# Kernel tuning notes

Measured on AMD Instinct MI355X. Metric: run time of the kernel, lower is better.

## Reference

```python
import jax, jax.numpy as jnp
import numpy as np


def setup_inputs() -> dict:
    key = jax.random.key(0)
    B, L, d_model, d_state, expand = 2, 2048, 1024, 16, 2
    d_inner = expand * d_model
    ks = jax.random.split(key, 8)
    s = lambda k, shape, scale: jax.random.normal(k, shape, dtype=jnp.float32) * scale
    x = s(ks[0], (B, L, d_model), 1.0)
    W_in = s(ks[1], (d_model, 2 * d_inner), 0.02)     # in_proj (no bias)
    W_delta = s(ks[2], (d_inner, d_inner), 0.02)      # delta_proj weight
    b_delta = s(ks[3], (d_inner,), 0.02)              # delta_proj bias
    W_B = s(ks[4], (d_inner, d_state), 0.02)          # B_proj (no bias)
    W_C = s(ks[5], (d_inner, d_state), 0.02)          # C_proj (no bias)
    # A_log = log(repeat(arange(1, d_state+1), 'n -> d n'))
    A_log = jnp.log(jnp.broadcast_to(
        jnp.arange(1, d_state + 1, dtype=jnp.float32), (d_inner, d_state)))
    D_param = jnp.ones((d_inner,), dtype=jnp.float32)
    W_out = s(ks[6], (d_inner, d_model), 0.02)        # out_proj (no bias)
    return dict(x=x, W_in=W_in, W_delta=W_delta, b_delta=b_delta,
                W_B=W_B, W_C=W_C, A_log=A_log, D_param=D_param, W_out=W_out)


def reference(x, W_in, W_delta, b_delta, W_B, W_C, A_log, D_param, W_out):
    d_inner = W_delta.shape[0]
    # in_proj then split into ssm branch (u) and gate (res)
    x_and_res = x @ W_in                       # (B, L, 2*d_inner)
    u, res = x_and_res[..., :d_inner], x_and_res[..., d_inner:]
    u = jax.nn.silu(u)                         # (B, L, d_inner)

    # input-dependent SSM parameters
    delta = jax.nn.softplus(u @ W_delta + b_delta)   # (B, L, d_inner)
    Bm = u @ W_B                                     # (B, L, d_state)
    Cm = u @ W_C                                     # (B, L, d_state)
    A = -jnp.exp(A_log)                              # (d_inner, d_state)

    def step(h, inp):
        d_t, B_t, C_t, u_t = inp  # (B,d), (B,n), (B,n), (B,d)
        dA = jnp.exp(d_t[..., None] * A)                          # (B,d,n)
        h = dA * h + d_t[..., None] * B_t[:, None, :] * u_t[..., None]
        y_t = jnp.einsum('bdn,bn->bd', h, C_t)
        return h, y_t

    Bsz = x.shape[0]
    h0 = jnp.zeros((Bsz, d_inner, A.shape[1]), dtype=x.dtype)
    xs = (jnp.swapaxes(delta, 0, 1), jnp.swapaxes(Bm, 0, 1),
          jnp.swapaxes(Cm, 0, 1), jnp.swapaxes(u, 0, 1))
    _, ys = jax.lax.scan(step, h0, xs)          # ys: (L, B, d_inner)
    y = jnp.swapaxes(ys, 0, 1) + u * D_param    # skip connection with D

    y = y * jax.nn.silu(res)                    # gating
    return y @ W_out                            # (B, L, d_model)
```

## Files before the change

### kernel.cpp

```cpp
#include <hip/hip_runtime.h>
#include <hip/hip_bf16.h>

typedef unsigned short ushort_t;
typedef __bf16 bf16x8 __attribute__((ext_vector_type(8)));
typedef float f32x4 __attribute__((ext_vector_type(4)));

typedef const void __attribute__((address_space(1)))* gas1_t;
typedef void __attribute__((address_space(3)))* las3_t;

#define L_SZ 2048
#define DI   2048
#define M_ROWS 4096
#define NC 32
#define TC 64

__device__ __forceinline__ float bf2f(ushort_t u){
  unsigned x = ((unsigned)u) << 16; float f; __builtin_memcpy(&f, &x, 4); return f;
}
__device__ __forceinline__ ushort_t f2bf(float f){
  __hip_bfloat16 h = __float2bfloat16(f);
  ushort_t u; __builtin_memcpy(&u, &h, 2); return u;
}
__device__ __forceinline__ float siluf(float x){ return x / (1.0f + __expf(-x)); }
__device__ __forceinline__ float softplusf(float x){
  return (x > 20.0f) ? x : log1pf(__expf(x));
}

__global__ __launch_bounds__(256) void k_prep(
    const float* __restrict__ W_in, const float* __restrict__ W_delta,
    const float* __restrict__ W_out, const float* __restrict__ W_B,
    const float* __restrict__ W_C, const float* __restrict__ x,
    ushort_t* __restrict__ W_inT, ushort_t* __restrict__ W_bigT,
    ushort_t* __restrict__ W_outT, ushort_t* __restrict__ xb)
{
  int t = blockIdx.x;
  if (t >= 14464){
    int r = 2080 + (t - 14464);
    uint4 z = make_uint4(0,0,0,0);
    *(uint4*)(W_bigT + (size_t)r * 2048 + threadIdx.x * 8) = z;
    return;
  }
  if (t >= 10368){
    size_t i = (size_t)(t - 10368) * 256 + threadIdx.x;
    float4 v = *(const float4*)(x + i * 4);
    ushort_t o[4] = { f2bf(v.x), f2bf(v.y), f2bf(v.z), f2bf(v.w) };
    *(uint2*)(xb + i * 4) = *(const uint2*)o;
    return;
  }
  const float* in; ushort_t* out; int R, C, tx, ty;
  if (t < 4096)      { in=W_in;    out=W_inT;  R=1024; C=4096; tx = t & 127; ty = t >> 7; }
  else if (t < 8192) { t -= 4096;  in=W_delta; out=W_bigT; R=2048; C=2048; tx = t & 63; ty = t >> 6; }
  else if (t < 10240){ t -= 8192;  in=W_out;   out=W_outT; R=2048; C=1024; tx = t & 31; ty = t >> 5; }
  else if (t < 10304){ t -= 10240; in=W_B;  out=W_bigT + (size_t)2048*2048; R=2048; C=16; tx=0; ty=t; }
  else               { t -= 10304; in=W_C;  out=W_bigT + (size_t)2064*2048; R=2048; C=16; tx=0; ty=t; }
  __shared__ ushort_t tile[32][33];
  int c0 = tx * 32, r0 = ty * 32;
  int xx = threadIdx.x & 31, yy = threadIdx.x >> 5;
  #pragma unroll
  for (int i = 0; i < 32; i += 8){
    int r = r0 + yy + i, c = c0 + xx;
    if (r < R && c < C) tile[yy + i][xx] = f2bf(in[(size_t)r * C + c]);
  }
  __syncthreads();
  #pragma unroll
  for (int i = 0; i < 32; i += 8){
    int c = c0 + yy + i, r = r0 + xx;
    if (r < R && c < C) out[(size_t)c * R + r] = tile[xx][yy + i];
  }
}

template<int BM, int BN, int TPB, int WR, int WC, int EPI, int MINW>
__global__ __launch_bounds__(TPB, MINW) void k_gemm2p(
    const ushort_t* __restrict__ A, int lda,
    const ushort_t* __restrict__ Bt, int ldb,
    void* __restrict__ Cout, int ldc,
    const float* __restrict__ bias,
    float* __restrict__ Bm, float* __restrict__ Cm, int K)
{
  constexpr int WM = BM / WR, WN = BN / WC;
  constexpr int MT = WM / 16, NT = WN / 16;
  constexpr int BUFSZ = (BM + BN) * 128;
  constexpr int ACH = BM * 8;
  constexpr int NISSUE = (BM + BN) * 8 / TPB;
  __shared__ __align__(16) char lds[2 * BUFSZ];
  const int tid  = threadIdx.x;
  const int wave = tid >> 6, lane = tid & 63;
  const int quad = lane >> 4, l16 = lane & 15;

  const int gx  = gridDim.x;
  const int nwg = gx * gridDim.y;
  const int bid = blockIdx.y * gx + blockIdx.x;
  const int cpx = nwg >> 3;
  const int wid = (bid & 7) * cpx + (bid >> 3);
  const int bx  = wid % gx, by = wid / gx;

  const int m_blk = by * BM, n_blk = bx * BN;
  const int wm = (wave / WC) * WM, wn = (wave % WC) * WN;

  f32x4 acc[MT][NT] = {};

  const ushort_t* gptr[NISSUE];
  char* lptr[NISSUE];
  #pragma unroll
  for (int i = 0; i < NISSUE; i++){
    int g = tid + i * TPB;
    if (g < ACH){
      int row = g >> 3, c = g & 7;
      gptr[i] = A + (size_t)(m_blk + row) * lda + ((c ^ (row & 7)) * 8);
    } else {
      int gb = g - ACH;
      int row = gb >> 3, c = gb & 7;
      gptr[i] = Bt + (size_t)(n_blk + row) * ldb + ((c ^ (row & 7)) * 8);
    }
    lptr[i] = lds + (size_t)g * 16;
  }

  const int xsw = (l16 & 7);
  const int NSTEP = K >> 6;

  #pragma unroll
  for (int i = 0; i < NISSUE; i++)
    __builtin_amdgcn_global_load_lds((gas1_t)(const void*)gptr[i], (las3_t)lptr[i], 16, 0, 0);
  __syncthreads();

  int cur = 0;
  for (int t = 0; t < NSTEP; ++t){
    if (t + 1 < NSTEP){
      const int nxt = (cur ^ 1) * BUFSZ;
      #pragma unroll
      for (int i = 0; i < NISSUE; i++)
        __builtin_amdgcn_global_load_lds((gas1_t)(const void*)(gptr[i] + (t + 1) * 64),
                                         (las3_t)(lptr[i] + nxt), 16, 0, 0);
    }
    const char* ldsA = lds + cur * BUFSZ;
    const char* ldsB = ldsA + BM * 128;
    #pragma unroll
    for (int s = 0; s < 2; s++){
      const int xa = ((s * 4 + quad) ^ xsw) * 16;
      bf16x8 af[MT], bfr[NT];
      #pragma unroll
      for (int i = 0; i < MT; i++)
        af[i]  = *(const bf16x8*)(ldsA + (wm + i * 16 + l16) * 128 + xa);
      #pragma unroll
      for (int i = 0; i < NT; i++)
        bfr[i] = *(const bf16x8*)(ldsB + (wn + i * 16 + l16) * 128 + xa);
      #pragma unroll
      for (int mt = 0; mt < MT; mt++)
        #pragma unroll
        for (int nt = 0; nt < NT; nt++)
          acc[mt][nt] = __builtin_amdgcn_mfma_f32_16x16x32_bf16(af[mt], bfr[nt], acc[mt][nt], 0, 0, 0);
    }
    __syncthreads();
    cur ^= 1;
  }

  #pragma unroll
  for (int mt = 0; mt < MT; mt++){
    #pragma unroll
    for (int nt = 0; nt < NT; nt++){
      #pragma unroll
      for (int r = 0; r < 4; r++){
        int m = m_blk + wm + mt * 16 + quad * 4 + r;
        int n = n_blk + wn + nt * 16 + l16;
        float v = acc[mt][nt][r];
        if (EPI == 0){
          ((float*)Cout)[(size_t)m * ldc + n] = v;
        } else if (EPI == 1){
          ((__hip_bfloat16*)Cout)[(size_t)m * ldc + n] = __float2bfloat16(siluf(v));
        } else {
          if (n < 2048)      ((ushort_t*)Cout)[(size_t)m * ldc + n] = f2bf(softplusf(v + bias[n]));
          else if (n < 2064) Bm[(size_t)m * 16 + (n - 2048)] = v;
          else if (n < 2080) Cm[(size_t)m * 16 + (n - 2064)] = v;
        }
      }
    }
  }
}

__device__ __forceinline__ void load_An(const float* A_log, int d, float* An){
  const float* ap = A_log + (size_t)d * 16;
  #pragma unroll
  for (int j = 0; j < 16; j += 4){
    float4 v = *(const float4*)(ap + j);
    An[j]   = -__expf(v.x);
    An[j+1] = -__expf(v.y);
    An[j+2] = -__expf(v.z);
    An[j+3] = -__expf(v.w);
  }
}

__global__ __launch_bounds__(256) void k_scan1(
    const ushort_t* __restrict__ delta, const ushort_t* __restrict__ U,
    const float* __restrict__ Bm, const float* __restrict__ A_log,
    float* __restrict__ q, float* __restrict__ S)
{
  __shared__ float ldsB[TC * 16];
  const int tid = threadIdx.x;
  const int ch  = blockIdx.x * 256 + tid;
  const int b   = ch >> 11, d = ch & 2047;
  const int c   = blockIdx.y;
  const int t0  = c * TC;
  {
    int tt = tid >> 2, n4 = (tid & 3) * 4;
    *(float4*)&ldsB[tt * 16 + n4] = *(const float4*)&Bm[((size_t)b * L_SZ + t0 + tt) * 16 + n4];
  }
  float An[16];
  load_An(A_log, d, An);
  __syncthreads();
  float h[16];
  #pragma unroll
  for (int j = 0; j < 16; j++) h[j] = 0.f;
  float Ssum = 0.f;
  const size_t row0 = (size_t)b * L_SZ + t0;
  for (int ti = 0; ti < TC; ti += 8){
    float dlt[8], uv[8];
    #pragma unroll
    for (int k = 0; k < 8; k++){
      size_t row = row0 + ti + k;
      dlt[k] = bf2f(delta[row * DI + d]);
      uv[k]  = bf2f(U[row * 4096 + d]);
    }
    #pragma unroll
    for (int k = 0; k < 8; k++){
      float du = dlt[k] * uv[k];
      Ssum += dlt[k];
      #pragma unroll
      for (int nn = 0; nn < 16; nn++)
        h[nn] = fmaf(__expf(dlt[k] * An[nn]), h[nn], du * ldsB[(ti + k) * 16 + nn]);
    }
  }
  size_t qb = ((size_t)c * M_ROWS + ch) * 16;
  #pragma unroll
  for (int j = 0; j < 16; j += 4)
    *(float4*)&q[qb + j] = make_float4(h[j], h[j+1], h[j+2], h[j+3]);
  S[(size_t)c * M_ROWS + ch] = Ssum;
}

__global__ __launch_bounds__(256) void k_scan_combine(
    const float* __restrict__ q, const float* __restrict__ S,
    const float* __restrict__ A_log, float* __restrict__ hin)
{
  int gid = blockIdx.x * 256 + threadIdx.x;
  int ch = gid >> 4, nn = gid & 15, d = ch & 2047;
  float An = -__expf(A_log[(size_t)d * 16 + nn]);
  float h = 0.f;
  for (int c = 0; c < NC; c++){
    size_t base = (size_t)c * M_ROWS + ch;
    hin[base * 16 + nn] = h;
    h = fmaf(__expf(An * S[base]), h, q[base * 16 + nn]);
  }
}

__global__ __launch_bounds__(256) void k_scan2(
    const ushort_t* __restrict__ delta, const ushort_t* __restrict__ U,
    const float* __restrict__ Bm, const float* __restrict__ Cm,
    const float* __restrict__ A_log, const float* __restrict__ Dpar,
    const float* __restrict__ hin, ushort_t* __restrict__ Y)
{
  __shared__ float ldsBC[TC * 16 * 2];
  const int tid = threadIdx.x;
  const int ch  = blockIdx.x * 256 + tid;
  const int b   = ch >> 11, d = ch & 2047;
  const int c   = blockIdx.y;
  const int t0  = c * TC;
  #pragma unroll
  for (int p = 0; p < 2; p++){
    int tt = (tid >> 3) + p * 32, n2 = (tid & 7) * 2;
    size_t gb = ((size_t)b * L_SZ + t0 + tt) * 16 + n2;
    float2 bv = *(const float2*)&Bm[gb];
    float2 cv = *(const float2*)&Cm[gb];
    float2* dst = (float2*)&ldsBC[(tt * 16 + n2) * 2];
    dst[0] = make_float2(bv.x, cv.x);
    dst[1] = make_float2(bv.y, cv.y);
  }
  float An[16];
  load_An(A_log, d, An);
  float Dv = Dpar[d];
  __syncthreads();
  float h[16];
  size_t hb = ((size_t)c * M_ROWS + ch) * 16;
  #pragma unroll
  for (int j = 0; j < 16; j += 4){
    float4 hv = *(const float4*)&hin[hb + j];
    h[j] = hv.x; h[j+1] = hv.y; h[j+2] = hv.z; h[j+3] = hv.w;
  }
  const size_t row0 = (size_t)b * L_SZ + t0;
  for (int ti = 0; ti < TC; ti += 8){
    float dlt[8], uv[8], sres[8];
    #pragma unroll
    for (int k = 0; k < 8; k++){
      size_t row = row0 + ti + k;
      dlt[k]  = bf2f(delta[row * DI + d]);
      uv[k]   = bf2f(U[row * 4096 + d]);
      sres[k] = bf2f(U[row * 4096 + 2048 + d]);
    }
    ushort_t yo[8];
    #pragma unroll
    for (int k = 0; k < 8; k++){
      float du = dlt[k] * uv[k];
      float y = 0.f;
      #pragma unroll
      for (int nn = 0; nn < 16; nn++){
        float2 bc = *(const float2*)&ldsBC[((ti + k) * 16 + nn) * 2];
        h[nn] = fmaf(__expf(dlt[k] * An[nn]), h[nn], du * bc.x);
        y = fmaf(h[nn], bc.y, y);
      }
      yo[k] = f2bf((y + uv[k] * Dv) * sres[k]);
    }
    #pragma unroll
    for (int k = 0; k < 8; k++)
      Y[(row0 + ti + k) * DI + d] = yo[k];
  }
}

extern "C" void kernel_launch(void* const* d_in, const int* in_sizes, int n_in,
                              void* d_out, int out_size, void* d_ws, size_t ws_size,
                              hipStream_t stream)
{
  const float* x       = (const float*)d_in[0];
  const float* W_in    = (const float*)d_in[1];
  const float* W_delta = (const float*)d_in[2];
  const float* b_delta = (const float*)d_in[3];
  const float* W_B     = (const float*)d_in[4];
  const float* W_C     = (const float*)d_in[5];
  const float* A_log   = (const float*)d_in[6];
  const float* D_par   = (const float*)d_in[7];
  const float* W_out   = (const float*)d_in[8];

  char* ws = (char*)d_ws;
  size_t off = 0;
  auto alloc = [&](size_t bytes){ char* p = ws + off; off += (bytes + 255) & ~(size_t)255; return p; };
  ushort_t* W_inT  = (ushort_t*)alloc((size_t)4096*1024*2);
  ushort_t* W_bigT = (ushort_t*)alloc((size_t)2304*2048*2);
  ushort_t* W_outT = (ushort_t*)alloc((size_t)1024*2048*2);
  ushort_t* xb     = (ushort_t*)alloc((size_t)4096*1024*2);
  ushort_t* U      = (ushort_t*)alloc((size_t)4096*4096*2);
  ushort_t* dl     = (ushort_t*)alloc((size_t)4096*2048*2);
  float*    Bm     = (float*)alloc((size_t)4096*16*4);
  float*    Cm     = (float*)alloc((size_t)4096*16*4);
  float*    qbuf   = (float*)alloc((size_t)NC*4096*16*4);
  float*    Sbuf   = (float*)alloc((size_t)NC*4096*4);
  float*    hin    = (float*)alloc((size_t)NC*4096*16*4);
  ushort_t* Y      = (ushort_t*)alloc((size_t)4096*2048*2);

  k_prep<<<dim3(14560),256,0,stream>>>(W_in, W_delta, W_out, W_B, W_C, x,
                                       W_inT, W_bigT, W_outT, xb);

  k_gemm2p<256,256,512,2,4,1,2><<<dim3(16,16),512,0,stream>>>(
      xb, 1024, W_inT, 1024, U, 4096, nullptr, nullptr, nullptr, 1024);

  k_gemm2p<128,64,256,2,2,2,3><<<dim3(34,32),256,0,stream>>>(
      U, 4096, W_bigT, 2048, dl, 2048, b_delta, Bm, Cm, 2048);

  k_scan1<<<dim3(16,NC),256,0,stream>>>(dl, U, Bm, A_log, qbuf, Sbuf);
  k_scan_combine<<<dim3(256),256,0,stream>>>(qbuf, Sbuf, A_log, hin);
  k_scan2<<<dim3(16,NC),256,0,stream>>>(dl, U, Bm, Cm, A_log, D_par, hin, Y);

  k_gemm2p<128,64,256,2,2,0,3><<<dim3(16,32),256,0,stream>>>(
      Y, 2048, W_outT, 2048, d_out, 1024, nullptr, nullptr, nullptr, 2048);
}
```

Measured before the change: 329.8 us.

## Triple-buffer LDS pipeline with explicit vmcnt waits for smaller GEMMs

Adds an NBUF template parameter to the GEMM kernel. The 3-buffer variant prefetches two K-steps ahead using global_load_lds and waits with a partial s_waitcnt vmcnt instead of a full syncthreads drain. The delta/B/C and output GEMMs switch to this path with min-waves lowered from 3 to 2. The goal is to hide global load latency better, at the cost of more LDS per block and possibly lower occupancy.

```diff
diff --git a/kernel.cpp b/kernel.cpp
--- a/kernel.cpp
+++ b/kernel.cpp
@@ -69,7 +69,7 @@
   }
 }
 
-template<int BM, int BN, int TPB, int WR, int WC, int EPI, int MINW>
+template<int BM, int BN, int TPB, int WR, int WC, int EPI, int MINW, int NBUF>
 __global__ __launch_bounds__(TPB, MINW) void k_gemm2p(
     const ushort_t* __restrict__ A, int lda,
     const ushort_t* __restrict__ Bt, int ldb,
@@ -82,7 +82,7 @@
   constexpr int BUFSZ = (BM + BN) * 128;
   constexpr int ACH = BM * 8;
   constexpr int NISSUE = (BM + BN) * 8 / TPB;
-  __shared__ __align__(16) char lds[2 * BUFSZ];
+  __shared__ __align__(16) char lds[NBUF * BUFSZ];
   const int tid  = threadIdx.x;
   const int wave = tid >> 6, lane = tid & 63;
   const int quad = lane >> 4, l16 = lane & 15;
@@ -118,40 +118,89 @@
   const int xsw = (l16 & 7);
   const int NSTEP = K >> 6;
 
-  #pragma unroll
-  for (int i = 0; i < NISSUE; i++)
-    __builtin_amdgcn_global_load_lds((gas1_t)(const void*)gptr[i], (las3_t)lptr[i], 16, 0, 0);
-  __syncthreads();
-
-  int cur = 0;
-  for (int t = 0; t < NSTEP; ++t){
-    if (t + 1 < NSTEP){
-      const int nxt = (cur ^ 1) * BUFSZ;
+  if constexpr (NBUF == 2){
+    #pragma unroll
+    for (int i = 0; i < NISSUE; i++)
+      __builtin_amdgcn_global_load_lds((gas1_t)(const void*)gptr[i], (las3_t)lptr[i], 16, 0, 0);
+    __syncthreads();
+
+    int cur = 0;
+    for (int t = 0; t < NSTEP; ++t){
+      if (t + 1 < NSTEP){
+        const int nxt = (cur ^ 1) * BUFSZ;
+        #pragma unroll
+        for (int i = 0; i < NISSUE; i++)
+          __builtin_amdgcn_global_load_lds((gas1_t)(const void*)(gptr[i] + (t + 1) * 64),
+                                           (las3_t)(lptr[i] + nxt), 16, 0, 0);
+      }
+      const char* ldsA = lds + cur * BUFSZ;
+      const char* ldsB = ldsA + BM * 128;
       #pragma unroll
-      for (int i = 0; i < NISSUE; i++)
-        __builtin_amdgcn_global_load_lds((gas1_t)(const void*)(gptr[i] + (t + 1) * 64),
-                                         (las3_t)(lptr[i] + nxt), 16, 0, 0);
-    }
-    const char* ldsA = lds + cur * BUFSZ;
-    const char* ldsB = ldsA + BM * 128;
-    #pragma unroll
-    for (int s = 0; s < 2; s++){
-      const int xa = ((s * 4 + quad) ^ xsw) * 16;
-      bf16x8 af[MT], bfr[NT];
+      for (int s = 0; s < 2; s++){
+        const int xa = ((s * 4 + quad) ^ xsw) * 16;
+        bf16x8 af[MT], bfr[NT];
+        #pragma unroll
+        for (int i = 0; i < MT; i++)
+          af[i]  = *(const bf16x8*)(ldsA + (wm + i * 16 + l16) * 128 + xa);
+        #pragma unroll
+        for (int i = 0; i < NT; i++)
+          bfr[i] = *(const bf16x8*)(ldsB + (wn + i * 16 + l16) * 128 + xa);
+        #pragma unroll
+        for (int mt = 0; mt < MT; mt++)
+          #pragma unroll
+          for (int nt = 0; nt < NT; nt++)
+            acc[mt][nt] = __builtin_amdgcn_mfma_f32_16x16x32_bf16(af[mt], bfr[nt], acc[mt][nt], 0, 0, 0);
+      }
+      __syncthreads();
+      cur ^= 1;
+    }
+  } else {
+    static_assert(NISSUE == 6, "vmcnt literal assumes 6 loads/step");
+    #pragma unroll
+    for (int i = 0; i < NISSUE; i++)
+      __builtin_amdgcn_global_load_lds((gas1_t)(const void*)gptr[i], (las3_t)lptr[i], 16, 0, 0);
+    #pragma unroll
+    for (int i = 0; i < NISSUE; i++)
+      __builtin_amdgcn_global_load_lds((gas1_t)(const void*)(gptr[i] + 64),
+                                       (las3_t)(lptr[i] + BUFSZ), 16, 0, 0);
+    asm volatile("s_waitcnt vmcnt(6)" ::: "memory");
+    __builtin_amdgcn_sched_barrier(0);
+    __builtin_amdgcn_s_barrier();
+    __builtin_amdgcn_sched_barrier(0);
+
+    int o0 = 0, o1 = BUFSZ, o2 = 2 * BUFSZ;
+    for (int t = 0; t < NSTEP; ++t){
+      if (t + 2 < NSTEP){
+        #pragma unroll
+        for (int i = 0; i < NISSUE; i++)
+          __builtin_amdgcn_global_load_lds((gas1_t)(const void*)(gptr[i] + (t + 2) * 64),
+                                           (las3_t)(lptr[i] + o2), 16, 0, 0);
+      }
+      const char* ldsA = lds + o0;
+      const char* ldsB = ldsA + BM * 128;
       #pragma unroll
-      for (int i = 0; i < MT; i++)
-        af[i]  = *(const bf16x8*)(ldsA + (wm + i * 16 + l16) * 128 + xa);
-      #pragma unroll
-      for (int i = 0; i < NT; i++)
-        bfr[i] = *(const bf16x8*)(ldsB + (wn + i * 16 + l16) * 128 + xa);
-      #pragma unroll
-      for (int mt = 0; mt < MT; mt++)
-        #pragma unroll
-        for (int nt = 0; nt < NT; nt++)
-          acc[mt][nt] = __builtin_amdgcn_mfma_f32_16x16x32_bf16(af[mt], bfr[nt], acc[mt][nt], 0, 0, 0);
-    }
-    __syncthreads();
-    cur ^= 1;
+      for (int s = 0; s < 2; s++){
+        const int xa = ((s * 4 + quad) ^ xsw) * 16;
+        bf16x8 af[MT], bfr[NT];
+        #pragma unroll
+        for (int i = 0; i < MT; i++)
+          af[i]  = *(const bf16x8*)(ldsA + (wm + i * 16 + l16) * 128 + xa);
+        #pragma unroll
+        for (int i = 0; i < NT; i++)
+          bfr[i] = *(const bf16x8*)(ldsB + (wn + i * 16 + l16) * 128 + xa);
+        #pragma unroll
+        for (int mt = 0; mt < MT; mt++)
+          #pragma unroll
+          for (int nt = 0; nt < NT; nt++)
+            acc[mt][nt] = __builtin_amdgcn_mfma_f32_16x16x32_bf16(af[mt], bfr[nt], acc[mt][nt], 0, 0, 0);
+      }
+      if (t + 2 < NSTEP){ asm volatile("s_waitcnt vmcnt(6)" ::: "memory"); }
+      else              { asm volatile("s_waitcnt vmcnt(0)" ::: "memory"); }
+      __builtin_amdgcn_sched_barrier(0);
+      __builtin_amdgcn_s_barrier();
+      __builtin_amdgcn_sched_barrier(0);
+      int tmp = o0; o0 = o1; o1 = o2; o2 = tmp;
+    }
   }
 
   #pragma unroll
@@ -346,16 +395,16 @@
   k_prep<<<dim3(14560),256,0,stream>>>(W_in, W_delta, W_out, W_B, W_C, x,
                                        W_inT, W_bigT, W_outT, xb);
 
-  k_gemm2p<256,256,512,2,4,1,2><<<dim3(16,16),512,0,stream>>>(
+  k_gemm2p<256,256,512,2,4,1,2,2><<<dim3(16,16),512,0,stream>>>(
       xb, 1024, W_inT, 1024, U, 4096, nullptr, nullptr, nullptr, 1024);
 
-  k_gemm2p<128,64,256,2,2,2,3><<<dim3(34,32),256,0,stream>>>(
+  k_gemm2p<128,64,256,2,2,2,2,3><<<dim3(34,32),256,0,stream>>>(
       U, 4096, W_bigT, 2048, dl, 2048, b_delta, Bm, Cm, 2048);
 
   k_scan1<<<dim3(16,NC),256,0,stream>>>(dl, U, Bm, A_log, qbuf, Sbuf);
   k_scan_combine<<<dim3(256),256,0,stream>>>(qbuf, Sbuf, A_log, hin);
   k_scan2<<<dim3(16,NC),256,0,stream>>>(dl, U, Bm, Cm, A_log, D_par, hin, Y);
 
-  k_gemm2p<128,64,256,2,2,0,3><<<dim3(16,32),256,0,stream>>>(
+  k_gemm2p<128,64,256,2,2,0,2,3><<<dim3(16,32),256,0,stream>>>(
       Y, 2048, W_outT, 2048, d_out, 1024, nullptr, nullptr, nullptr, 2048);
 }
```

Result: slower. 366.6 us (+11.1%).
